# Kernel optimization log

Measured on AMD Instinct MI355X. Metric: run time of the kernel, lower is better.

The kernel has to match this reference:

```python
import jax, jax.numpy as jnp
import numpy as np

B, S, D = 1, 2048, 2048
H = 16
Q_LORA = 1536
KV_LORA = 512
NOPE = 128
ROPE = 64
VD = 128
QHD = NOPE + ROPE  # 192
THETA = 50000.0
EPS = 1e-6


def rmsnorm(x, w, eps=EPS):
    xf = x.astype(jnp.float32)
    var = jnp.mean(xf * xf, axis=-1, keepdims=True)
    return (w * (xf * jax.lax.rsqrt(var + eps)).astype(x.dtype))


def rotate_half(x):
    x1, x2 = jnp.split(x, 2, axis=-1)
    return jnp.concatenate([-x2, x1], axis=-1)


def deinterleave(x):
    # view(..., d//2, 2).transpose(-1,-2).reshape(..., d): [x0,x2,...,x1,x3,...]
    b, h, s, d = x.shape
    return x.reshape(b, h, s, d // 2, 2).swapaxes(-1, -2).reshape(b, h, s, d)


def setup_inputs() -> dict:
    key = jax.random.key(0)
    ks = jax.random.split(key, 8)
    sc = 0.02
    return {
        "hidden_states": jax.random.normal(ks[0], (B, S, D), jnp.float32),
        "position_ids": jnp.broadcast_to(jnp.arange(S, dtype=jnp.int32), (B, S)),
        "q_a_w": jax.random.normal(ks[1], (Q_LORA, D), jnp.float32) * sc,
        "q_a_ln_w": jnp.ones((Q_LORA,), jnp.float32),
        "q_b_w": jax.random.normal(ks[2], (H * QHD, Q_LORA), jnp.float32) * sc,
        "kv_a_w": jax.random.normal(ks[3], (KV_LORA + ROPE, D), jnp.float32) * sc,
        "kv_a_ln_w": jnp.ones((KV_LORA,), jnp.float32),
        "kv_b_w": jax.random.normal(ks[4], (H * (NOPE + VD), KV_LORA), jnp.float32) * sc,
        "o_w": jax.random.normal(ks[5], (D, H * VD), jnp.float32) * sc,
    }


def reference(hidden_states, position_ids, q_a_w, q_a_ln_w, q_b_w, kv_a_w, kv_a_ln_w, kv_b_w, o_w):
    bsz, q_len, _ = hidden_states.shape
    # low-rank Q: q_b(rmsnorm(q_a(x)))
    q = rmsnorm(hidden_states @ q_a_w.T, q_a_ln_w) @ q_b_w.T
    q = q.reshape(bsz, q_len, H, QHD).transpose(0, 2, 1, 3)  # [b,h,s,192]
    q_nope, q_pe = q[..., :NOPE], q[..., NOPE:]
    # compressed KV + shared rope key
    ckv = hidden_states @ kv_a_w.T  # [b,s,512+64]
    compressed_kv, k_pe = ckv[..., :KV_LORA], ckv[..., KV_LORA:]
    k_pe = k_pe.reshape(bsz, q_len, 1, ROPE).transpose(0, 2, 1, 3)  # [b,1,s,64]
    kv = rmsnorm(compressed_kv, kv_a_ln_w) @ kv_b_w.T
    kv = kv.reshape(bsz, q_len, H, NOPE + VD).transpose(0, 2, 1, 3)
    k_nope, value_states = kv[..., :NOPE], kv[..., NOPE:]
    # rotary cache
    inv_freq = 1.0 / (THETA ** (jnp.arange(0, ROPE, 2, dtype=jnp.float32) / ROPE))
    t = jnp.arange(q_len, dtype=jnp.float32)
    freqs = jnp.outer(t, inv_freq)
    emb = jnp.concatenate([freqs, freqs], axis=-1)  # [s,64]
    cos = jnp.cos(emb)[position_ids][:, None]  # [b,1,s,64]
    sin = jnp.sin(emb)[position_ids][:, None]
    q_pe = deinterleave(q_pe)
    k_pe = deinterleave(k_pe)
    q_pe = q_pe * cos + rotate_half(q_pe) * sin
    k_pe = k_pe * cos + rotate_half(k_pe) * sin
    query_states = jnp.concatenate([q_nope, q_pe], axis=-1)  # [b,h,s,192]
    key_states = jnp.concatenate([k_nope, jnp.broadcast_to(k_pe, (bsz, H, q_len, ROPE))], axis=-1)
    scale = QHD ** (-0.5)
    scores = jnp.einsum('bhqd,bhkd->bhqk', query_states, key_states) * scale
    causal = jnp.tril(jnp.ones((q_len, q_len), bool))
    scores = jnp.where(causal, scores, jnp.finfo(scores.dtype).min)
    attn = jax.nn.softmax(scores, axis=-1)
    out = jnp.einsum('bhqk,bhkd->bhqd', attn, value_states)  # [b,h,s,128]
    out = out.transpose(0, 2, 1, 3).reshape(bsz, q_len, H * VD)
    return out @ o_w.T
```

## Files before the change

### kernel.cpp

```cpp
#include <hip/hip_runtime.h>
#include <hip/hip_bf16.h>
#include <cmath>

#define S_LEN 2048
#define D_MODEL 2048
#define N_HEADS 16
#define Q_LORA 1536
#define KV_LORA 512
#define NOPE 128
#define ROPE_D 64
#define VD 128
#define QHD 192
#define AC_W 2112

typedef __attribute__((ext_vector_type(8))) short bf16x8;
typedef __attribute__((ext_vector_type(4))) float f32x4;
typedef __attribute__((ext_vector_type(4))) unsigned short u16x4;

static __device__ __forceinline__ unsigned short f2u(float x) {
  union { float f; unsigned u; } v; v.f = x;
  unsigned r = v.u + 0x7fffu + ((v.u >> 16) & 1u);
  return (unsigned short)(r >> 16);
}
static __device__ __forceinline__ unsigned short f2u_fast(float x) {
  union { float f; unsigned u; } v; v.f = x;
  return (unsigned short)((v.u + 0x8000u) >> 16);
}
static __device__ __forceinline__ float u2f(unsigned short x) {
  union { unsigned u; float f; } v; v.u = ((unsigned)x) << 16;
  return v.f;
}

#define AS1 __attribute__((address_space(1)))
#define AS3 __attribute__((address_space(3)))
static __device__ __forceinline__ void gload_lds16(const unsigned short* g, unsigned short* l) {
  __builtin_amdgcn_global_load_lds((const AS1 unsigned int*)g, (AS3 unsigned int*)l, 16, 0, 0);
}

__global__ __launch_bounds__(256) void conv_bf16(const float* __restrict__ src,
                                                 unsigned short* __restrict__ dst,
                                                 int n4, float scale) {
  for (int i = blockIdx.x * 256 + threadIdx.x; i < n4; i += gridDim.x * 256) {
    const float4 v = ((const float4*)src)[i];
    u16x4 o;
    o[0] = f2u(v.x * scale); o[1] = f2u(v.y * scale);
    o[2] = f2u(v.z * scale); o[3] = f2u(v.w * scale);
    ((u16x4*)dst)[i] = o;
  }
}

__global__ __launch_bounds__(256) void conv_stage1(const float* __restrict__ hidden,
                                                   const float* __restrict__ qaw,
                                                   const float* __restrict__ kvaw,
                                                   unsigned short* __restrict__ Hb,
                                                   unsigned short* __restrict__ wbuf) {
  const int nH = (S_LEN * D_MODEL) / 4;
  const int nQ = (Q_LORA * D_MODEL) / 4;
  const int nT = nH + nQ + ((KV_LORA + ROPE_D) * D_MODEL) / 4;
  for (int i = blockIdx.x * 256 + threadIdx.x; i < nT; i += gridDim.x * 256) {
    float4 v;
    unsigned short* dst;
    int o;
    if (i < nH) {
      v = ((const float4*)hidden)[i]; dst = Hb; o = i;
    } else {
      o = i - nH;
      v = (o < nQ) ? ((const float4*)qaw)[o] : ((const float4*)kvaw)[o - nQ];
      dst = wbuf;
    }
    u16x4 u;
    u[0] = f2u(v.x); u[1] = f2u(v.y); u[2] = f2u(v.z); u[3] = f2u(v.w);
    ((u16x4*)dst)[o] = u;
  }
}

__global__ __launch_bounds__(256) void conv_stage2(const float* __restrict__ qbw,
                                                   const float* __restrict__ kvbsrc,
                                                   unsigned short* __restrict__ wbuf,
                                                   unsigned short* __restrict__ kvbw,
                                                   float qscale) {
  const int nQB = (N_HEADS * QHD * Q_LORA) / 4;
  const int nT = nQB + (N_HEADS * 256 * KV_LORA) / 4;
  for (int i = blockIdx.x * 256 + threadIdx.x; i < nT; i += gridDim.x * 256) {
    u16x4 u;
    if (i < nQB) {
      const float4 v = ((const float4*)qbw)[i];
      u[0] = f2u(v.x * qscale); u[1] = f2u(v.y * qscale);
      u[2] = f2u(v.z * qscale); u[3] = f2u(v.w * qscale);
      ((u16x4*)wbuf)[i] = u;
    } else {
      const int o = i - nQB;
      const float4 v = ((const float4*)kvbsrc)[o];
      u[0] = f2u(v.x); u[1] = f2u(v.y); u[2] = f2u(v.z); u[3] = f2u(v.w);
      ((u16x4*)kvbw)[o] = u;
    }
  }
}

template <int MODE>
__global__ __launch_bounds__(256) void gemm_mfma(const unsigned short* __restrict__ A,
                                                 const unsigned short* __restrict__ W,
                                                 void* __restrict__ Cv,
                                                 unsigned short* __restrict__ C2,
                                                 int N, int K) {
  __shared__ unsigned short As[2][8192];
  __shared__ unsigned short Ws[2][4096];
  const int tid = threadIdx.x;
  const int wave = tid >> 6, lane = tid & 63;
  const int col16 = lane & 15, g = lane >> 4;
  const int arow = blockIdx.y * 128, wrow = blockIdx.x * 64;
  const int wm = (wave >> 1) * 64, wn = (wave & 1) * 32;

  const unsigned short* gA[4];
  const unsigned short* gW[2];
  int dA[4], dW[2];
#pragma unroll
  for (int i = 0; i < 4; ++i) {
    const int c = i * 256 + tid;
    const int r = c >> 3, sl = c & 7;
    gA[i] = A + (size_t)(arow + r) * K + (sl ^ (r & 7)) * 8;
    dA[i] = c * 8;
  }
#pragma unroll
  for (int i = 0; i < 2; ++i) {
    const int c = i * 256 + tid;
    const int r = c >> 3, sl = c & 7;
    gW[i] = W + (size_t)(wrow + r) * K + (sl ^ (r & 7)) * 8;
    dW[i] = c * 8;
  }

  f32x4 acc[4][2];
#pragma unroll
  for (int i = 0; i < 4; ++i)
#pragma unroll
    for (int j = 0; j < 2; ++j) acc[i][j] = (f32x4){0.f, 0.f, 0.f, 0.f};

#pragma unroll
  for (int i = 0; i < 4; ++i) gload_lds16(gA[i], &As[0][dA[i]]);
#pragma unroll
  for (int i = 0; i < 2; ++i) gload_lds16(gW[i], &Ws[0][dW[i]]);

  int cur = 0;
  for (int k0 = 0; k0 < K; k0 += 64) {
    __syncthreads();
    if (k0 + 64 < K) {
      const int b = cur ^ 1, kk = k0 + 64;
#pragma unroll
      for (int i = 0; i < 4; ++i) gload_lds16(gA[i] + kk, &As[b][dA[i]]);
#pragma unroll
      for (int i = 0; i < 2; ++i) gload_lds16(gW[i] + kk, &Ws[b][dW[i]]);
    }
#pragma unroll
    for (int kh = 0; kh < 2; ++kh) {
      bf16x8 af[4], bfr[2];
#pragma unroll
      for (int i = 0; i < 4; ++i) {
        const int row = wm + i * 16 + col16;
        af[i] = *(const bf16x8*)(&As[cur][row * 64 + (((kh * 4 + g) ^ (row & 7)) * 8)]);
      }
#pragma unroll
      for (int j = 0; j < 2; ++j) {
        const int row = wn + j * 16 + col16;
        bfr[j] = *(const bf16x8*)(&Ws[cur][row * 64 + (((kh * 4 + g) ^ (row & 7)) * 8)]);
      }
#pragma unroll
      for (int i = 0; i < 4; ++i)
#pragma unroll
        for (int j = 0; j < 2; ++j)
          acc[i][j] = __builtin_amdgcn_mfma_f32_16x16x32_bf16(af[i], bfr[j], acc[i][j], 0, 0, 0);
    }
    cur ^= 1;
  }

#pragma unroll
  for (int i = 0; i < 4; ++i)
#pragma unroll
    for (int j = 0; j < 2; ++j) {
      const int col = wrow + wn + j * 16 + col16;
      const int row0 = arow + wm + i * 16 + g * 4;
      if constexpr (MODE == 0) {
#pragma unroll
        for (int r = 0; r < 4; ++r)
          ((float*)Cv)[(size_t)(row0 + r) * N + col] = acc[i][j][r];
      } else if constexpr (MODE == 1) {
#pragma unroll
        for (int r = 0; r < 4; ++r)
          ((unsigned short*)Cv)[(size_t)(row0 + r) * N + col] = f2u(acc[i][j][r]);
      } else {
        const int hh = col >> 8, d = col & 255;
        if (d < NOPE) {
#pragma unroll
          for (int r = 0; r < 4; ++r)
            C2[((size_t)hh * S_LEN + row0 + r) * QHD + d] = f2u(acc[i][j][r]);
        } else {
          const int dv = d - NOPE;
          const int p0 = ((row0 & 15) >> 2) * 8 + ((row0 >> 4) & 1) * 4;
          u16x4 w4;
#pragma unroll
          for (int r = 0; r < 4; ++r) w4[r] = f2u(acc[i][j][r]);
          *(uint2*)((unsigned short*)Cv + ((size_t)hh * VD + dv) * S_LEN + (row0 & ~31) + p0) =
              __builtin_bit_cast(uint2, w4);
        }
      }
    }
}

__global__ __launch_bounds__(256) void rmsnorm2_kernel(const float* __restrict__ ac,
                                                       const float* __restrict__ wq,
                                                       const float* __restrict__ wkv,
                                                       unsigned short* __restrict__ qan,
                                                       unsigned short* __restrict__ ckvn) {
  const int row = blockIdx.x;
  const bool kv = blockIdx.y != 0;
  const float* x = ac + (size_t)row * AC_W + (kv ? Q_LORA : 0);
  const float* w = kv ? wkv : wq;
  unsigned short* dst = kv ? (ckvn + (size_t)row * KV_LORA) : (qan + (size_t)row * Q_LORA);
  const int dim = kv ? KV_LORA : Q_LORA;
  float ss = 0.f;
  for (int i = threadIdx.x; i < dim; i += 256) {
    float v = x[i];
    ss += v * v;
  }
#pragma unroll
  for (int off = 32; off; off >>= 1) ss += __shfl_xor(ss, off);
  __shared__ float red[4];
  const int wv = threadIdx.x >> 6, ln = threadIdx.x & 63;
  if (ln == 0) red[wv] = ss;
  __syncthreads();
  const float tot = red[0] + red[1] + red[2] + red[3];
  const float scale = rsqrtf(tot / (float)dim + 1e-6f);
  for (int i = threadIdx.x; i < dim; i += 256) {
    dst[i] = f2u(w[i] * (x[i] * scale));
  }
}

__global__ void rope_kernel(unsigned short* __restrict__ q, const float* __restrict__ ac,
                            unsigned short* __restrict__ Kb, const int* __restrict__ pos_ids) {
  const int s = blockIdx.x;
  const int j = threadIdx.x;
  const float t = (float)pos_ids[s];
  const float invf = powf(50000.0f, -(float)(2 * j) / 64.0f);
  const float ang = t * invf;
  const float c = cosf(ang), sn = sinf(ang);
  for (int h = 0; h < N_HEADS; ++h) {
    unsigned short* base = q + (size_t)s * (N_HEADS * QHD) + h * QHD + NOPE;
    const float x0 = u2f(base[2 * j]), x1 = u2f(base[2 * j + 1]);
    __syncthreads();
    base[j] = f2u(x0 * c - x1 * sn);
    base[32 + j] = f2u(x1 * c + x0 * sn);
    __syncthreads();
  }
  const float* kb = ac + (size_t)s * AC_W + 2048;
  const unsigned short r0 = f2u(kb[2 * j] * c - kb[2 * j + 1] * sn);
  const unsigned short r1 = f2u(kb[2 * j + 1] * c + kb[2 * j] * sn);
#pragma unroll
  for (int h = 0; h < N_HEADS; ++h) {
    unsigned short* kd = Kb + ((size_t)h * S_LEN + s) * QHD + NOPE;
    kd[j] = r0;
    kd[32 + j] = r1;
  }
}

__global__ __launch_bounds__(256, 4) void flash_attn(const unsigned short* __restrict__ Q,
                                                     const unsigned short* __restrict__ Kb,
                                                     const unsigned short* __restrict__ Vt,
                                                     unsigned short* __restrict__ Pb,
                                                     float2* __restrict__ mlb) {
  __shared__ unsigned short Ks[2][32 * QHD];
  __shared__ unsigned short Vs[2][VD * 32];
  const int tid = threadIdx.x;
  const int wave = tid >> 6, lane = tid & 63;
  const int g = lane >> 4, col = lane & 15;
  const int lin = (int)blockIdx.x;
  const int h = ((lin & 7) << 1) | ((lin >> 3) & 1);
  const int s = (lin >> 4) & 1;
  const int z = lin >> 5;
  int t;
  if (z < 8) t = 31 - z;
  else if (z < 16) t = z - 8;
  else if (z < 24) t = 39 - z;
  else t = z - 16;
  const int qw = t * 64 + wave * 16;
  const int qr = qw + col;

  bf16x8 qf[6];
  {
    const unsigned short* qrow = Q + (size_t)qr * (N_HEADS * QHD) + h * QHD + g * 8;
#pragma unroll
    for (int i = 0; i < 6; ++i) qf[i] = *(const bf16x8*)(qrow + i * 32);
  }

  const unsigned short* KbH = Kb + (size_t)h * S_LEN * QHD;
  const unsigned short* VtH = Vt + (size_t)h * VD * S_LEN;

  int eK[3], eV[2];
#pragma unroll
  for (int i = 0; i < 3; ++i) {
    const int c = i * 256 + tid;
    const int r = c / 24, sl = c - r * 24;
    eK[i] = r * QHD + (((sl & 24) | ((sl & 7) ^ (r & 7)))) * 8;
  }
#pragma unroll
  for (int i = 0; i < 2; ++i) {
    const int c = i * 256 + tid;
    const int d = c >> 2, sl = c & 3;
    eV[i] = d * S_LEN + ((sl ^ (d & 3))) * 8;
  }

  f32x4 o[8];
#pragma unroll
  for (int i = 0; i < 8; ++i) o[i] = (f32x4){0.f, 0.f, 0.f, 0.f};
  float m = -1e30f, l = 0.f;

  const int nT = t + 1;

  {
    const unsigned short* kp = KbH + (size_t)s * 32 * QHD;
    const unsigned short* vp = VtH + s * 32;
#pragma unroll
    for (int i = 0; i < 3; ++i) gload_lds16(kp + eK[i], &Ks[0][(i * 256 + tid) * 8]);
#pragma unroll
    for (int i = 0; i < 2; ++i) gload_lds16(vp + eV[i], &Vs[0][(i * 256 + tid) * 8]);
  }

  int xK[6];
#pragma unroll
  for (int i = 0; i < 6; ++i) xK[i] = ((4 * i + g) ^ (col & 7)) * 8;
  const int rbK = col * QHD;
  const int xV = (g ^ (col & 3)) * 8;
  const int rbV = col * 32;

  for (int it = 0; it < nT; ++it) {
    __syncthreads();
    if (it + 1 < nT) {
      const int jn = 2 * (it + 1) + s;
      const unsigned short* kp = KbH + (size_t)jn * 32 * QHD;
      const unsigned short* vp = VtH + jn * 32;
      const int b = (it + 1) & 1;
#pragma unroll
      for (int i = 0; i < 3; ++i) gload_lds16(kp + eK[i], &Ks[b][(i * 256 + tid) * 8]);
#pragma unroll
      for (int i = 0; i < 2; ++i) gload_lds16(vp + eV[i], &Vs[b][(i * 256 + tid) * 8]);
    }
    const int k0 = 32 * (2 * it + s);
    if (k0 <= qw + 15) {
      const unsigned short* Ksc = Ks[it & 1];
      const unsigned short* Vsc = Vs[it & 1];

      f32x4 c0 = (f32x4){0.f, 0.f, 0.f, 0.f}, c1 = (f32x4){0.f, 0.f, 0.f, 0.f};
      __builtin_amdgcn_s_setprio(1);
#pragma unroll
      for (int dt = 0; dt < 6; ++dt) {
        const bf16x8 a0 = *(const bf16x8*)(Ksc + rbK + xK[dt]);
        const bf16x8 a1 = *(const bf16x8*)(Ksc + rbK + 16 * QHD + xK[dt]);
        c0 = __builtin_amdgcn_mfma_f32_16x16x32_bf16(a0, qf[dt], c0, 0, 0, 0);
        c1 = __builtin_amdgcn_mfma_f32_16x16x32_bf16(a1, qf[dt], c1, 0, 0, 0);
      }
      __builtin_amdgcn_s_setprio(0);

      if (k0 + 31 > qw) {
#pragma unroll
        for (int r = 0; r < 4; ++r) {
          const int kk = k0 + 4 * g + r;
          if (kk > qr) c0[r] = -1e30f;
          if (kk + 16 > qr) c1[r] = -1e30f;
        }
      }
      float bm = fmaxf(fmaxf(fmaxf(c0[0], c0[1]), fmaxf(c0[2], c0[3])),
                       fmaxf(fmaxf(c1[0], c1[1]), fmaxf(c1[2], c1[3])));
      bm = fmaxf(bm, __shfl_xor(bm, 16));
      bm = fmaxf(bm, __shfl_xor(bm, 32));
      const bool skip = __all(bm <= m + 8.f);
      const float mn = skip ? m : fmaxf(m, bm);
      float ps = 0.f;
      bf16x8 pb;
#pragma unroll
      for (int r = 0; r < 4; ++r) {
        const float p0 = exp2f(c0[r] - mn);
        const float p1 = exp2f(c1[r] - mn);
        ps += p0 + p1;
        pb[r] = (short)f2u_fast(p0);
        pb[4 + r] = (short)f2u_fast(p1);
      }
      ps += __shfl_xor(ps, 16);
      ps += __shfl_xor(ps, 32);
      if (skip) {
        l += ps;
      } else {
        const float corr = exp2f(m - mn);
        l = l * corr + ps;
        m = mn;
#pragma unroll
        for (int i = 0; i < 8; ++i) {
          o[i][0] *= corr; o[i][1] *= corr; o[i][2] *= corr; o[i][3] *= corr;
        }
      }
      __builtin_amdgcn_s_setprio(1);
#pragma unroll
      for (int db = 0; db < 8; ++db) {
        const bf16x8 va = *(const bf16x8*)(Vsc + db * 512 + rbV + xV);
        o[db] = __builtin_amdgcn_mfma_f32_16x16x32_bf16(va, pb, o[db], 0, 0, 0);
      }
      __builtin_amdgcn_s_setprio(0);
    }
  }

  unsigned short* pr = Pb + (((size_t)qr * 2 + s) * N_HEADS + h) * VD;
#pragma unroll
  for (int db = 0; db < 8; ++db) {
    u16x4 w4;
#pragma unroll
    for (int r = 0; r < 4; ++r) w4[r] = f2u(o[db][r]);
    *(uint2*)(pr + db * 16 + 4 * g) = __builtin_bit_cast(uint2, w4);
  }
  if (g == 0) mlb[((size_t)qr * 2 + s) * N_HEADS + h] = make_float2(m, l);
}

__global__ __launch_bounds__(256) void combine2(const unsigned short* __restrict__ Pb,
                                                const float2* __restrict__ mlb,
                                                unsigned short* __restrict__ outb) {
  const int idx = blockIdx.x * 256 + threadIdx.x;
  const int d8 = idx & 15, hq = idx >> 4;
  const int h = hq & 15, q = hq >> 4;
  const float2 a = mlb[((size_t)q * 2 + 0) * N_HEADS + h];
  const float2 b = mlb[((size_t)q * 2 + 1) * N_HEADS + h];
  const float M = fmaxf(a.x, b.x);
  float wA = exp2f(a.x - M), wB = exp2f(b.x - M);
  const float inv = 1.f / (wA * a.y + wB * b.y);
  wA *= inv; wB *= inv;
  const bf16x8 v0 = *(const bf16x8*)(Pb + (((size_t)q * 2 + 0) * N_HEADS + h) * VD + d8 * 8);
  const bf16x8 v1 = *(const bf16x8*)(Pb + (((size_t)q * 2 + 1) * N_HEADS + h) * VD + d8 * 8);
  u16x4 o0, o1;
#pragma unroll
  for (int e = 0; e < 4; ++e) {
    o0[e] = f2u(u2f((unsigned short)v0[e]) * wA + u2f((unsigned short)v1[e]) * wB);
    o1[e] = f2u(u2f((unsigned short)v0[4 + e]) * wA + u2f((unsigned short)v1[4 + e]) * wB);
  }
  unsigned short* dst = outb + ((size_t)q * N_HEADS + h) * VD + d8 * 8;
  *(uint2*)(dst) = __builtin_bit_cast(uint2, o0);
  *(uint2*)(dst + 4) = __builtin_bit_cast(uint2, o1);
}

extern "C" void kernel_launch(void* const* d_in, const int* in_sizes, int n_in,
                              void* d_out, int out_size, void* d_ws, size_t ws_size,
                              hipStream_t stream) {
  const float* hidden    = (const float*)d_in[0];
  const int*   pos       = (const int*)d_in[1];
  const float* q_a_w     = (const float*)d_in[2];
  const float* q_a_ln_w  = (const float*)d_in[3];
  const float* q_b_w     = (const float*)d_in[4];
  const float* kv_a_w    = (const float*)d_in[5];
  const float* kv_a_ln_w = (const float*)d_in[6];
  const float* kv_b_w    = (const float*)d_in[7];
  const float* o_w       = (const float*)d_in[8];
  float* out = (float*)d_out;
  (void)in_sizes; (void)n_in; (void)out_size; (void)ws_size;

  char* base = (char*)d_ws;
  unsigned short* qbuf  = (unsigned short*)(base);
  unsigned short* Pbuf  = (unsigned short*)(base + 12582912);
  float*          ac    = (float*)(base + 29360128);
  unsigned short* qan   = (unsigned short*)(base + 46661632);
  float2*         mlb   = (float2*)(base + 46661632);
  unsigned short* ckvn  = (unsigned short*)(base + 52953088);
  unsigned short* Hb    = (unsigned short*)(base + 55050240);
  unsigned short* Vt    = (unsigned short*)(base + 55050240);
  unsigned short* wbuf  = (unsigned short*)(base + 63438848);
  unsigned short* attnb = (unsigned short*)(base + 72876032);
  unsigned short* kvbw  = (unsigned short*)(base + 72876032);
  unsigned short* Kb    = (unsigned short*)(base + 81264640);

  const dim3 b256(256);
  const float qscale = 0.07216878364870323f * 1.4426950408889634f;

  conv_stage1<<<2048, b256, 0, stream>>>(hidden, q_a_w, kv_a_w, Hb, wbuf);

  gemm_mfma<0><<<dim3(AC_W / 64, S_LEN / 128), b256, 0, stream>>>(Hb, wbuf, ac, nullptr, AC_W, D_MODEL);

  rmsnorm2_kernel<<<dim3(S_LEN, 2), b256, 0, stream>>>(ac, q_a_ln_w, kv_a_ln_w, qan, ckvn);

  conv_stage2<<<2048, b256, 0, stream>>>(q_b_w, kv_b_w, wbuf, kvbw, qscale);

  gemm_mfma<1><<<dim3(N_HEADS * QHD / 64, S_LEN / 128), b256, 0, stream>>>(qan, wbuf, qbuf, nullptr, N_HEADS * QHD, Q_LORA);

  gemm_mfma<2><<<dim3(N_HEADS * 256 / 64, S_LEN / 128), b256, 0, stream>>>(ckvn, kvbw, Vt, Kb, N_HEADS * 256, KV_LORA);

  rope_kernel<<<S_LEN, 32, 0, stream>>>(qbuf, ac, Kb, pos);

  flash_attn<<<dim3(1024), b256, 0, stream>>>(qbuf, Kb, Vt, Pbuf, mlb);
  combine2<<<2048, b256, 0, stream>>>(Pbuf, mlb, attnb);

  conv_bf16<<<2048, b256, 0, stream>>>(o_w, wbuf, (D_MODEL * N_HEADS * VD) / 4, 1.f);
  gemm_mfma<0><<<dim3(D_MODEL / 64, S_LEN / 128), b256, 0, stream>>>(attnb, wbuf, out, nullptr, D_MODEL, N_HEADS * VD);
}
```

Measured before the change: 195.9 us.

## Fuse Q and KV up-projection GEMMs into one launch and store latent projections as bf16

Combines the q_b and kv_b GEMMs into a single kernel whose flat grid dispatches blocks to either problem, removing a launch and letting both fill the GPU together. The first projection output is now written as bf16 instead of fp32, halving its write and read traffic, and rmsnorm reads it with 16-byte vector loads. Rope reads the k_pe slice from the bf16 buffer. This adds rounding of the pre-norm activations and the rope key to bf16.

```diff
diff --git a/kernel.cpp b/kernel.cpp
--- a/kernel.cpp
+++ b/kernel.cpp
@@ -101,7 +101,6 @@
 __global__ __launch_bounds__(256) void gemm_mfma(const unsigned short* __restrict__ A,
                                                  const unsigned short* __restrict__ W,
                                                  void* __restrict__ Cv,
-                                                 unsigned short* __restrict__ C2,
                                                  int N, int K) {
   __shared__ unsigned short As[2][8192];
   __shared__ unsigned short Ws[2][4096];
@@ -178,48 +177,148 @@
     for (int j = 0; j < 2; ++j) {
       const int col = wrow + wn + j * 16 + col16;
       const int row0 = arow + wm + i * 16 + g * 4;
-      if constexpr (MODE == 0) {
+#pragma unroll
+      for (int r = 0; r < 4; ++r) {
+        if constexpr (MODE == 0)
+          ((float*)Cv)[(size_t)(row0 + r) * N + col] = acc[i][j][r];
+        else
+          ((unsigned short*)Cv)[(size_t)(row0 + r) * N + col] = f2u(acc[i][j][r]);
+      }
+    }
+}
+
+__global__ __launch_bounds__(256) void gemm_qkv(const unsigned short* __restrict__ qan,
+                                                const unsigned short* __restrict__ wq,
+                                                unsigned short* __restrict__ qbuf,
+                                                const unsigned short* __restrict__ ckvn,
+                                                const unsigned short* __restrict__ wkv,
+                                                unsigned short* __restrict__ Kb,
+                                                unsigned short* __restrict__ Vt) {
+  __shared__ unsigned short As[2][8192];
+  __shared__ unsigned short Ws[2][4096];
+  const int tid = threadIdx.x;
+  const int wave = tid >> 6, lane = tid & 63;
+  const int col16 = lane & 15, g = lane >> 4;
+  const int bid = (int)blockIdx.x;
+  const bool isQ = bid < 768;
+  int bx, by;
+  if (isQ) { bx = bid % 48; by = bid / 48; }
+  else { const int r = bid - 768; bx = r & 63; by = r >> 6; }
+  const int K = isQ ? Q_LORA : KV_LORA;
+  const unsigned short* A = isQ ? qan : ckvn;
+  const unsigned short* W = isQ ? wq : wkv;
+  const int arow = by * 128, wrow = bx * 64;
+  const int wm = (wave >> 1) * 64, wn = (wave & 1) * 32;
+
+  const unsigned short* gA[4];
+  const unsigned short* gW[2];
+  int dA[4], dW[2];
+#pragma unroll
+  for (int i = 0; i < 4; ++i) {
+    const int c = i * 256 + tid;
+    const int r = c >> 3, sl = c & 7;
+    gA[i] = A + (size_t)(arow + r) * K + (sl ^ (r & 7)) * 8;
+    dA[i] = c * 8;
+  }
+#pragma unroll
+  for (int i = 0; i < 2; ++i) {
+    const int c = i * 256 + tid;
+    const int r = c >> 3, sl = c & 7;
+    gW[i] = W + (size_t)(wrow + r) * K + (sl ^ (r & 7)) * 8;
+    dW[i] = c * 8;
+  }
+
+  f32x4 acc[4][2];
+#pragma unroll
+  for (int i = 0; i < 4; ++i)
+#pragma unroll
+    for (int j = 0; j < 2; ++j) acc[i][j] = (f32x4){0.f, 0.f, 0.f, 0.f};
+
+#pragma unroll
+  for (int i = 0; i < 4; ++i) gload_lds16(gA[i], &As[0][dA[i]]);
+#pragma unroll
+  for (int i = 0; i < 2; ++i) gload_lds16(gW[i], &Ws[0][dW[i]]);
+
+  int cur = 0;
+  for (int k0 = 0; k0 < K; k0 += 64) {
+    __syncthreads();
+    if (k0 + 64 < K) {
+      const int b = cur ^ 1, kk = k0 + 64;
+#pragma unroll
+      for (int i = 0; i < 4; ++i) gload_lds16(gA[i] + kk, &As[b][dA[i]]);
+#pragma unroll
+      for (int i = 0; i < 2; ++i) gload_lds16(gW[i] + kk, &Ws[b][dW[i]]);
+    }
+#pragma unroll
+    for (int kh = 0; kh < 2; ++kh) {
+      bf16x8 af[4], bfr[2];
+#pragma unroll
+      for (int i = 0; i < 4; ++i) {
+        const int row = wm + i * 16 + col16;
+        af[i] = *(const bf16x8*)(&As[cur][row * 64 + (((kh * 4 + g) ^ (row & 7)) * 8)]);
+      }
+#pragma unroll
+      for (int j = 0; j < 2; ++j) {
+        const int row = wn + j * 16 + col16;
+        bfr[j] = *(const bf16x8*)(&Ws[cur][row * 64 + (((kh * 4 + g) ^ (row & 7)) * 8)]);
+      }
+#pragma unroll
+      for (int i = 0; i < 4; ++i)
+#pragma unroll
+        for (int j = 0; j < 2; ++j)
+          acc[i][j] = __builtin_amdgcn_mfma_f32_16x16x32_bf16(af[i], bfr[j], acc[i][j], 0, 0, 0);
+    }
+    cur ^= 1;
+  }
+
+#pragma unroll
+  for (int i = 0; i < 4; ++i)
+#pragma unroll
+    for (int j = 0; j < 2; ++j) {
+      const int col = wrow + wn + j * 16 + col16;
+      const int row0 = arow + wm + i * 16 + g * 4;
+      if (isQ) {
 #pragma unroll
         for (int r = 0; r < 4; ++r)
-          ((float*)Cv)[(size_t)(row0 + r) * N + col] = acc[i][j][r];
-      } else if constexpr (MODE == 1) {
-#pragma unroll
-        for (int r = 0; r < 4; ++r)
-          ((unsigned short*)Cv)[(size_t)(row0 + r) * N + col] = f2u(acc[i][j][r]);
+          qbuf[(size_t)(row0 + r) * (N_HEADS * QHD) + col] = f2u(acc[i][j][r]);
       } else {
         const int hh = col >> 8, d = col & 255;
         if (d < NOPE) {
 #pragma unroll
           for (int r = 0; r < 4; ++r)
-            C2[((size_t)hh * S_LEN + row0 + r) * QHD + d] = f2u(acc[i][j][r]);
+            Kb[((size_t)hh * S_LEN + row0 + r) * QHD + d] = f2u(acc[i][j][r]);
         } else {
           const int dv = d - NOPE;
           const int p0 = ((row0 & 15) >> 2) * 8 + ((row0 >> 4) & 1) * 4;
           u16x4 w4;
 #pragma unroll
           for (int r = 0; r < 4; ++r) w4[r] = f2u(acc[i][j][r]);
-          *(uint2*)((unsigned short*)Cv + ((size_t)hh * VD + dv) * S_LEN + (row0 & ~31) + p0) =
+          *(uint2*)(Vt + ((size_t)hh * VD + dv) * S_LEN + (row0 & ~31) + p0) =
               __builtin_bit_cast(uint2, w4);
         }
       }
     }
 }
 
-__global__ __launch_bounds__(256) void rmsnorm2_kernel(const float* __restrict__ ac,
+__global__ __launch_bounds__(256) void rmsnorm2_kernel(const unsigned short* __restrict__ ac,
                                                        const float* __restrict__ wq,
                                                        const float* __restrict__ wkv,
                                                        unsigned short* __restrict__ qan,
                                                        unsigned short* __restrict__ ckvn) {
   const int row = blockIdx.x;
   const bool kv = blockIdx.y != 0;
-  const float* x = ac + (size_t)row * AC_W + (kv ? Q_LORA : 0);
+  const unsigned short* x = ac + (size_t)row * AC_W + (kv ? Q_LORA : 0);
   const float* w = kv ? wkv : wq;
   unsigned short* dst = kv ? (ckvn + (size_t)row * KV_LORA) : (qan + (size_t)row * Q_LORA);
   const int dim = kv ? KV_LORA : Q_LORA;
   float ss = 0.f;
-  for (int i = threadIdx.x; i < dim; i += 256) {
-    float v = x[i];
-    ss += v * v;
+  for (int i0 = threadIdx.x * 8; i0 < dim; i0 += 2048) {
+    const bf16x8 v = *(const bf16x8*)(x + i0);
+#pragma unroll
+    for (int e = 0; e < 8; ++e) {
+      const float f = u2f((unsigned short)v[e]);
+      ss += f * f;
+    }
   }
 #pragma unroll
   for (int off = 32; off; off >>= 1) ss += __shfl_xor(ss, off);
@@ -229,12 +328,20 @@
   __syncthreads();
   const float tot = red[0] + red[1] + red[2] + red[3];
   const float scale = rsqrtf(tot / (float)dim + 1e-6f);
-  for (int i = threadIdx.x; i < dim; i += 256) {
-    dst[i] = f2u(w[i] * (x[i] * scale));
-  }
-}
-
-__global__ void rope_kernel(unsigned short* __restrict__ q, const float* __restrict__ ac,
+  for (int i0 = threadIdx.x * 8; i0 < dim; i0 += 2048) {
+    const bf16x8 v = *(const bf16x8*)(x + i0);
+    u16x4 o0, o1;
+#pragma unroll
+    for (int e = 0; e < 4; ++e) {
+      o0[e] = f2u(w[i0 + e] * (u2f((unsigned short)v[e]) * scale));
+      o1[e] = f2u(w[i0 + 4 + e] * (u2f((unsigned short)v[4 + e]) * scale));
+    }
+    *(uint2*)(dst + i0) = __builtin_bit_cast(uint2, o0);
+    *(uint2*)(dst + i0 + 4) = __builtin_bit_cast(uint2, o1);
+  }
+}
+
+__global__ void rope_kernel(unsigned short* __restrict__ q, const unsigned short* __restrict__ ac,
                             unsigned short* __restrict__ Kb, const int* __restrict__ pos_ids) {
   const int s = blockIdx.x;
   const int j = threadIdx.x;
@@ -250,9 +357,10 @@
     base[32 + j] = f2u(x1 * c + x0 * sn);
     __syncthreads();
   }
-  const float* kb = ac + (size_t)s * AC_W + 2048;
-  const unsigned short r0 = f2u(kb[2 * j] * c - kb[2 * j + 1] * sn);
-  const unsigned short r1 = f2u(kb[2 * j + 1] * c + kb[2 * j] * sn);
+  const unsigned short* kb = ac + (size_t)s * AC_W + 2048;
+  const float kb0 = u2f(kb[2 * j]), kb1 = u2f(kb[2 * j + 1]);
+  const unsigned short r0 = f2u(kb0 * c - kb1 * sn);
+  const unsigned short r1 = f2u(kb1 * c + kb0 * sn);
 #pragma unroll
   for (int h = 0; h < N_HEADS; ++h) {
     unsigned short* kd = Kb + ((size_t)h * S_LEN + s) * QHD + NOPE;
@@ -459,7 +567,7 @@
   char* base = (char*)d_ws;
   unsigned short* qbuf  = (unsigned short*)(base);
   unsigned short* Pbuf  = (unsigned short*)(base + 12582912);
-  float*          ac    = (float*)(base + 29360128);
+  unsigned short* acb   = (unsigned short*)(base + 29360128);
   unsigned short* qan   = (unsigned short*)(base + 46661632);
   float2*         mlb   = (float2*)(base + 46661632);
   unsigned short* ckvn  = (unsigned short*)(base + 52953088);
@@ -475,21 +583,19 @@
 
   conv_stage1<<<2048, b256, 0, stream>>>(hidden, q_a_w, kv_a_w, Hb, wbuf);
 
-  gemm_mfma<0><<<dim3(AC_W / 64, S_LEN / 128), b256, 0, stream>>>(Hb, wbuf, ac, nullptr, AC_W, D_MODEL);
-
-  rmsnorm2_kernel<<<dim3(S_LEN, 2), b256, 0, stream>>>(ac, q_a_ln_w, kv_a_ln_w, qan, ckvn);
+  gemm_mfma<1><<<dim3(AC_W / 64, S_LEN / 128), b256, 0, stream>>>(Hb, wbuf, acb, AC_W, D_MODEL);
+
+  rmsnorm2_kernel<<<dim3(S_LEN, 2), b256, 0, stream>>>(acb, q_a_ln_w, kv_a_ln_w, qan, ckvn);
 
   conv_stage2<<<2048, b256, 0, stream>>>(q_b_w, kv_b_w, wbuf, kvbw, qscale);
 
-  gemm_mfma<1><<<dim3(N_HEADS * QHD / 64, S_LEN / 128), b256, 0, stream>>>(qan, wbuf, qbuf, nullptr, N_HEADS * QHD, Q_LORA);
-
-  gemm_mfma<2><<<dim3(N_HEADS * 256 / 64, S_LEN / 128), b256, 0, stream>>>(ckvn, kvbw, Vt, Kb, N_HEADS * 256, KV_LORA);
-
-  rope_kernel<<<S_LEN, 32, 0, stream>>>(qbuf, ac, Kb, pos);
+  gemm_qkv<<<dim3(1792), b256, 0, stream>>>(qan, wbuf, qbuf, ckvn, kvbw, Kb, Vt);
+
+  rope_kernel<<<S_LEN, 32, 0, stream>>>(qbuf, acb, Kb, pos);
 
   flash_attn<<<dim3(1024), b256, 0, stream>>>(qbuf, Kb, Vt, Pbuf, mlb);
   combine2<<<2048, b256, 0, stream>>>(Pbuf, mlb, attnb);
 
   conv_bf16<<<2048, b256, 0, stream>>>(o_w, wbuf, (D_MODEL * N_HEADS * VD) / 4, 1.f);
-  gemm_mfma<0><<<dim3(D_MODEL / 64, S_LEN / 128), b256, 0, stream>>>(attnb, wbuf, out, nullptr, D_MODEL, N_HEADS * VD);
-}
+  gemm_mfma<0><<<dim3(D_MODEL / 64, S_LEN / 128), b256, 0, stream>>>(attnb, wbuf, out, D_MODEL, N_HEADS * VD);
+}
```

Result: faster. 189.3 us (-3.4%).
